# Performance work log

Hardware: AMD Instinct MI355X
Metric: run time of the kernel (lower is better)

The kernel has to match this reference:

```python
import jax, jax.numpy as jnp
import numpy as np

C_MSA, C_Z, C_HID, N_HEADS = 64, 128, 32, 8
INF = 1e8
EPS = 1e-5

def layer_norm(x, g, b):
    mu = jnp.mean(x, axis=-1, keepdims=True)
    var = jnp.var(x, axis=-1, keepdims=True)
    return (x - mu) * jax.lax.rsqrt(var + EPS) * g + b

def setup_inputs() -> dict:
    key = jax.random.key(0)
    ks = jax.random.split(key, 8)
    n_seq, n_res = 256, 512
    m = jax.random.normal(ks[0], (n_seq, n_res, C_MSA), dtype=jnp.float32)
    z = jax.random.normal(ks[1], (n_res, n_res, C_Z), dtype=jnp.float32)
    msa_mask = jnp.ones((n_seq, n_res), dtype=jnp.float32)
    z_mask = jnp.ones((n_res, n_res), dtype=jnp.float32)
    hc = N_HEADS * C_HID
    s_v = 1.0 / np.sqrt(C_MSA)
    W_v = jax.random.normal(ks[2], (hc, C_MSA), dtype=jnp.float32) * s_v
    W_g = jax.random.normal(ks[3], (hc, C_MSA), dtype=jnp.float32) * s_v  # 'gating' init is zeros; random for testing
    W_b = jax.random.normal(ks[4], (N_HEADS, C_Z), dtype=jnp.float32) * (1.0 / np.sqrt(C_Z))
    W_o = jax.random.normal(ks[5], (C_MSA, hc), dtype=jnp.float32) * (1.0 / np.sqrt(hc))
    ln_m_g = jnp.ones((C_MSA,), jnp.float32); ln_m_b = jnp.zeros((C_MSA,), jnp.float32)
    ln_z_g = jnp.ones((C_Z,), jnp.float32); ln_z_b = jnp.zeros((C_Z,), jnp.float32)
    return {"m": m, "z": z, "msa_mask": msa_mask, "z_mask": z_mask,
            "ln_m_g": ln_m_g, "ln_m_b": ln_m_b, "W_v": W_v, "W_g": W_g,
            "ln_z_g": ln_z_g, "ln_z_b": ln_z_b, "W_b": W_b, "W_o": W_o}

def reference(m, z, msa_mask, z_mask, ln_m_g, ln_m_b, W_v, W_g, ln_z_g, ln_z_b, W_b, W_o):
    n_seq, n_res, _ = m.shape
    m_ln = layer_norm(m, ln_m_g, ln_m_b)                      # [s, i, c_msa]
    v = (m_ln @ W_v.T).reshape(n_seq, n_res, N_HEADS, C_HID)  # [s, j, h, c]
    g = jax.nn.sigmoid(m_ln @ W_g.T).reshape(n_seq, n_res, N_HEADS, C_HID)
    b = layer_norm(z, ln_z_g, ln_z_b) @ W_b.T                 # [i, j, h]
    b = b + INF * (z_mask[..., None] - 1.0)
    v = v * msa_mask[..., None, None]
    w = jax.nn.softmax(b, axis=-2)                            # softmax over j
    # o[s,i,h,c] = sum_j v[s,j,h,c] * w[i,j,h]  (no broadcast materialization)
    o = g * jnp.einsum('sjhc,ijh->sihc', v, w)
    out = o.reshape(n_seq, n_res, N_HEADS * C_HID) @ W_o.T    # [s, i, c_msa]
    return out
```

## Files before the change

### kernel.cpp

```cpp
#include <hip/hip_runtime.h>
#include <stdint.h>


typedef unsigned short u16;
typedef unsigned int u32;
typedef __attribute__((ext_vector_type(4))) float f32x4;
typedef __attribute__((ext_vector_type(8))) short bf16x8;

#define INF8 1e8f

__device__ __forceinline__ u16 f2bf(float f) {
  u32 u = __float_as_uint(f);
  u = u + 0x7fffu + ((u >> 16) & 1u);
  return (u16)(u >> 16);
}
__device__ __forceinline__ float bf2f(u16 h) {
  return __uint_as_float(((u32)h) << 16);
}

#define GLD_LDS16(gp, lp) __builtin_amdgcn_global_load_lds(                 \
    (__attribute__((address_space(1))) const void*)(gp),                    \
    (__attribute__((address_space(3))) void*)(lp), 16, 0, 0)

__global__ __launch_bounds__(256) void k1_bias_softmax(
    const float* __restrict__ z, const float* __restrict__ z_mask,
    const float* __restrict__ gzp, const float* __restrict__ bzp,
    const float* __restrict__ W_b, u16* __restrict__ w_out)
{
  const int i = blockIdx.x;
  const int t = threadIdx.x;
  __shared__ float zn[32][133];
  __shared__ float bl[8][512];
  __shared__ float wb[8][128];
  __shared__ float gz[128], bz[128];
  for (int idx = t; idx < 1024; idx += 256) wb[idx >> 7][idx & 127] = W_b[idx];
  if (t < 128) { gz[t] = gzp[t]; bz[t] = bzp[t]; }
  __syncthreads();

  const int jl = t >> 3;
  const int part = t & 7;
  const int h = t >> 5, jj = t & 31;

  for (int chunk = 0; chunk < 16; ++chunk) {
    const float* zrow = z + ((size_t)i * 512 + chunk * 32 + jl) * 128;
    f32x4 v[4];
    float s = 0.f, sq = 0.f;
#pragma unroll
    for (int q = 0; q < 4; ++q) {
      v[q] = *reinterpret_cast<const f32x4*>(zrow + 4 * (part + 8 * q));
#pragma unroll
      for (int e = 0; e < 4; ++e) { s += v[q][e]; sq += v[q][e] * v[q][e]; }
    }
#pragma unroll
    for (int msk = 1; msk < 8; msk <<= 1) {
      s += __shfl_xor(s, msk, 8);
      sq += __shfl_xor(sq, msk, 8);
    }
    float mean = s * (1.f / 128.f);
    float rstd = rsqrtf(sq * (1.f / 128.f) - mean * mean + 1e-5f);
#pragma unroll
    for (int q = 0; q < 4; ++q) {
      int k0 = 4 * (part + 8 * q);
#pragma unroll
      for (int e = 0; e < 4; ++e) {
        int k = k0 + e;
        zn[jl][k] = (v[q][e] - mean) * rstd * gz[k] + bz[k];
      }
    }
    __syncthreads();
    {
      float acc = 0.f;
#pragma unroll 8
      for (int k = 0; k < 128; ++k) acc += zn[jj][k] * wb[h][k];
      float zm = z_mask[(size_t)i * 512 + chunk * 32 + jj];
      bl[h][chunk * 32 + jj] = acc + INF8 * (zm - 1.f);
    }
    __syncthreads();
  }
  {
    const int l = t & 31;
    float vals[16];
    float mx = -3.4e38f;
#pragma unroll
    for (int q = 0; q < 16; ++q) { vals[q] = bl[h][l + 32 * q]; mx = fmaxf(mx, vals[q]); }
#pragma unroll
    for (int msk = 1; msk < 32; msk <<= 1) mx = fmaxf(mx, __shfl_xor(mx, msk, 32));
    float sum = 0.f;
#pragma unroll
    for (int q = 0; q < 16; ++q) { vals[q] = __expf(vals[q] - mx); sum += vals[q]; }
#pragma unroll
    for (int msk = 1; msk < 32; msk <<= 1) sum += __shfl_xor(sum, msk, 32);
    float inv = 1.f / sum;
    u16* wrow = w_out + ((size_t)h * 512 + i) * 512;
#pragma unroll
    for (int q = 0; q < 16; ++q) wrow[l + 32 * q] = f2bf(vals[q] * inv);
  }
}

__global__ __launch_bounds__(256) void k2_vg(
    const float* __restrict__ m, const float* __restrict__ msa_mask,
    const float* __restrict__ gmp, const float* __restrict__ bmp,
    const float* __restrict__ W_v, const float* __restrict__ W_g,
    u16* __restrict__ vT, u16* __restrict__ g_out)
{
  const int jt = blockIdx.x, s = blockIdx.y;
  const int j0 = jt * 128;
  const int t = threadIdx.x;
  const int lane = t & 63, wid = t >> 6;
  __shared__ u16 bt[128][80];
  __shared__ float gk[64], bk[64];
  if (t < 64) { gk[t] = gmp[t]; bk[t] = bmp[t]; }
  __syncthreads();

  if (t < 128) {
    const float* mrow = m + ((size_t)s * 512 + j0 + t) * 64;
    f32x4 v[16];
    float s1 = 0.f, s2 = 0.f;
#pragma unroll
    for (int q = 0; q < 16; ++q) {
      v[q] = *reinterpret_cast<const f32x4*>(mrow + 4 * q);
#pragma unroll
      for (int e = 0; e < 4; ++e) { s1 += v[q][e]; s2 += v[q][e] * v[q][e]; }
    }
    float mean = s1 * (1.f / 64.f);
    float rstd = rsqrtf(s2 * (1.f / 64.f) - mean * mean + 1e-5f);
#pragma unroll
    for (int q = 0; q < 16; ++q) {
      int k0 = q * 4;
      u32 p0 = (u32)f2bf((v[q][0] - mean) * rstd * gk[k0]     + bk[k0])
             | ((u32)f2bf((v[q][1] - mean) * rstd * gk[k0 + 1] + bk[k0 + 1]) << 16);
      u32 p1 = (u32)f2bf((v[q][2] - mean) * rstd * gk[k0 + 2] + bk[k0 + 2])
             | ((u32)f2bf((v[q][3] - mean) * rstd * gk[k0 + 3] + bk[k0 + 3]) << 16);
      *reinterpret_cast<u32*>(&bt[t][k0]) = p0;
      *reinterpret_cast<u32*>(&bt[t][k0 + 2]) = p1;
    }
  }

  const float* Wsrc = (wid < 2) ? W_v : W_g;
  const int row0 = (wid & 1) * 128;
  const int r16 = lane & 15, kg = lane >> 4;
  bf16x8 afrag[8][2];
#pragma unroll
  for (int mf = 0; mf < 8; ++mf) {
    int row = row0 + mf * 16 + r16;
#pragma unroll
    for (int kf = 0; kf < 2; ++kf) {
      int k = kf * 32 + kg * 8;
      f32x4 x0 = *reinterpret_cast<const f32x4*>(Wsrc + row * 64 + k);
      f32x4 x1 = *reinterpret_cast<const f32x4*>(Wsrc + row * 64 + k + 4);
      bf16x8 a;
      a[0] = (short)f2bf(x0[0]); a[1] = (short)f2bf(x0[1]);
      a[2] = (short)f2bf(x0[2]); a[3] = (short)f2bf(x0[3]);
      a[4] = (short)f2bf(x1[0]); a[5] = (short)f2bf(x1[1]);
      a[6] = (short)f2bf(x1[2]); a[7] = (short)f2bf(x1[3]);
      afrag[mf][kf] = a;
    }
  }
  __syncthreads();

  for (int nc = 0; nc < 8; ++nc) {
    bf16x8 b0 = *reinterpret_cast<const bf16x8*>(&bt[nc * 16 + r16][kg * 8]);
    bf16x8 b1 = *reinterpret_cast<const bf16x8*>(&bt[nc * 16 + r16][32 + kg * 8]);
    f32x4 acc[8];
#pragma unroll
    for (int mf = 0; mf < 8; ++mf) acc[mf] = (f32x4){0.f, 0.f, 0.f, 0.f};
#pragma unroll
    for (int mf = 0; mf < 8; ++mf) {
      acc[mf] = __builtin_amdgcn_mfma_f32_16x16x32_bf16(afrag[mf][0], b0, acc[mf], 0, 0, 0);
      acc[mf] = __builtin_amdgcn_mfma_f32_16x16x32_bf16(afrag[mf][1], b1, acc[mf], 0, 0, 0);
    }
    const int colj = j0 + nc * 16 + r16;
    if (wid < 2) {
      float mask = msa_mask[(size_t)s * 512 + colj];
#pragma unroll
      for (int mf = 0; mf < 8; ++mf) {
#pragma unroll
        for (int r = 0; r < 4; ++r) {
          int hcrow = row0 + mf * 16 + kg * 4 + r;
          int hh = hcrow >> 5, cc = hcrow & 31;
          vT[((size_t)hh * 8192 + s * 32 + cc) * 512 + colj] = f2bf(acc[mf][r] * mask);
        }
      }
    } else {
#pragma unroll
      for (int mf = 0; mf < 8; ++mf) {
        int hcrow0 = row0 + mf * 16 + kg * 4;
        u16 pk0 = f2bf(1.f / (1.f + __expf(-acc[mf][0])));
        u16 pk1 = f2bf(1.f / (1.f + __expf(-acc[mf][1])));
        u16 pk2 = f2bf(1.f / (1.f + __expf(-acc[mf][2])));
        u16 pk3 = f2bf(1.f / (1.f + __expf(-acc[mf][3])));
        u32* dst = reinterpret_cast<u32*>(g_out + ((size_t)s * 512 + colj) * 256 + hcrow0);
        dst[0] = (u32)pk0 | ((u32)pk1 << 16);
        dst[1] = (u32)pk2 | ((u32)pk3 << 16);
      }
    }
  }
}

__global__ __launch_bounds__(256) void k3_einsum(
    const u16* __restrict__ w_buf, const u16* __restrict__ vT,
    float* __restrict__ O)
{
  const int nt = blockIdx.x, mt = blockIdx.y, h = blockIdx.z;
  const int t = threadIdx.x, lane = t & 63, wid = t >> 6;
  const int Mbase = mt * 128, Nbase = nt * 128;
  __shared__ u16 at[128 * 32];
  __shared__ u16 btl[128 * 32];
  const u16* Ag = w_buf + (size_t)h * 512 * 512;
  const u16* Bg = vT + (size_t)h * 8192 * 512;
  const int wr = wid >> 1, wc = wid & 1;
  const int r16 = lane & 15, kg = lane >> 4;
  const int srow = lane >> 2, scol = (lane & 3) * 8;
  f32x4 acc[4][4];
#pragma unroll
  for (int ii = 0; ii < 4; ++ii)
#pragma unroll
    for (int jj2 = 0; jj2 < 4; ++jj2) acc[ii][jj2] = (f32x4){0.f, 0.f, 0.f, 0.f};

  for (int kt = 0; kt < 16; ++kt) {
    const int k0 = kt * 32;
#pragma unroll
    for (int q = 0; q < 2; ++q) {
      const int rbase = wid * 32 + q * 16;
      GLD_LDS16(Ag + (size_t)(Mbase + rbase + srow) * 512 + k0 + scol, at + rbase * 32);
      GLD_LDS16(Bg + (size_t)(Nbase + rbase + srow) * 512 + k0 + scol, btl + rbase * 32);
    }
    __syncthreads();
    bf16x8 av[4], bv[4];
#pragma unroll
    for (int mf = 0; mf < 4; ++mf)
      av[mf] = *reinterpret_cast<const bf16x8*>(&at[(wr * 64 + mf * 16 + r16) * 32 + kg * 8]);
#pragma unroll
    for (int nf = 0; nf < 4; ++nf)
      bv[nf] = *reinterpret_cast<const bf16x8*>(&btl[(wc * 64 + nf * 16 + r16) * 32 + kg * 8]);
#pragma unroll
    for (int mf = 0; mf < 4; ++mf)
#pragma unroll
      for (int nf = 0; nf < 4; ++nf)
        acc[mf][nf] = __builtin_amdgcn_mfma_f32_16x16x32_bf16(av[mf], bv[nf], acc[mf][nf], 0, 0, 0);
    __syncthreads();
  }
  float* Obase = O + (size_t)h * 512 * 8192;
#pragma unroll
  for (int mf = 0; mf < 4; ++mf) {
#pragma unroll
    for (int r = 0; r < 4; ++r) {
      const int irow = Mbase + wr * 64 + mf * 16 + kg * 4 + r;
#pragma unroll
      for (int nf = 0; nf < 4; ++nf) {
        const int n = Nbase + wc * 64 + nf * 16 + r16;
        Obase[(size_t)irow * 8192 + n] = acc[mf][nf][r];
      }
    }
  }
}

__global__ __launch_bounds__(256) void k4_out(
    const float* __restrict__ O, const u16* __restrict__ g_buf,
    const float* __restrict__ W_o, float* __restrict__ out)
{
  const int st = blockIdx.x, i = blockIdx.y;
  const int s0 = st * 64;
  const int t = threadIdx.x, lane = t & 63, wid = t >> 6;
  __shared__ u16 Al[64][264];
  __shared__ u16 Wl[64][264];
  for (int idx = t; idx < 64 * 256; idx += 256) {
    int row = idx >> 8, col = idx & 255;
    Wl[row][col] = f2bf(W_o[idx]);
  }
  {
    const int hh = t >> 5, cc = t & 31;
    const float* Op = O + ((size_t)hh * 512 + i) * 8192 + (size_t)s0 * 32 + cc;
    const u16* gp = g_buf + ((size_t)s0 * 512 + i) * 256 + t;
#pragma unroll 4
    for (int sl = 0; sl < 64; ++sl) {
      float ov = Op[sl * 32];
      float gv = bf2f(gp[sl * 131072]);
      Al[sl][t] = f2bf(ov * gv);
    }
  }
  __syncthreads();

  const int r16 = lane & 15, kg = lane >> 4;
  f32x4 acc[4];
#pragma unroll
  for (int nf = 0; nf < 4; ++nf) acc[nf] = (f32x4){0.f, 0.f, 0.f, 0.f};
#pragma unroll
  for (int kf = 0; kf < 8; ++kf) {
    bf16x8 a = *reinterpret_cast<const bf16x8*>(&Al[wid * 16 + r16][kf * 32 + kg * 8]);
#pragma unroll
    for (int nf = 0; nf < 4; ++nf) {
      bf16x8 b = *reinterpret_cast<const bf16x8*>(&Wl[nf * 16 + r16][kf * 32 + kg * 8]);
      acc[nf] = __builtin_amdgcn_mfma_f32_16x16x32_bf16(a, b, acc[nf], 0, 0, 0);
    }
  }
#pragma unroll
  for (int nf = 0; nf < 4; ++nf) {
#pragma unroll
    for (int r = 0; r < 4; ++r) {
      int srow = wid * 16 + kg * 4 + r;
      int cm = nf * 16 + r16;
      out[((size_t)(s0 + srow) * 512 + i) * 64 + cm] = acc[nf][r];
    }
  }
}

extern "C" void kernel_launch(void* const* d_in, const int* in_sizes, int n_in,
                              void* d_out, int out_size, void* d_ws, size_t ws_size,
                              hipStream_t stream) {
  const float* m        = (const float*)d_in[0];
  const float* z        = (const float*)d_in[1];
  const float* msa_mask = (const float*)d_in[2];
  const float* z_mask   = (const float*)d_in[3];
  const float* ln_m_g   = (const float*)d_in[4];
  const float* ln_m_b   = (const float*)d_in[5];
  const float* W_v      = (const float*)d_in[6];
  const float* W_g      = (const float*)d_in[7];
  const float* ln_z_g   = (const float*)d_in[8];
  const float* ln_z_b   = (const float*)d_in[9];
  const float* W_b      = (const float*)d_in[10];
  const float* W_o      = (const float*)d_in[11];
  float* out = (float*)d_out;

  char* ws = (char*)d_ws;
  u16*   w_buf = (u16*)(ws);
  u16*   vT    = (u16*)(ws + (4u << 20));
  u16*   g_buf = (u16*)(ws + (68u << 20));
  float* O     = (float*)(ws + (132u << 20));

  k1_bias_softmax<<<dim3(512), dim3(256), 0, stream>>>(z, z_mask, ln_z_g, ln_z_b, W_b, w_buf);
  k2_vg<<<dim3(4, 256), dim3(256), 0, stream>>>(m, msa_mask, ln_m_g, ln_m_b, W_v, W_g, vT, g_buf);
  k3_einsum<<<dim3(64, 4, 8), dim3(256), 0, stream>>>(w_buf, vT, O);
  k4_out<<<dim3(4, 512), dim3(256), 0, stream>>>(O, g_buf, W_o, out);
}
```

Before: 438.4 us.

## Rewrite pipeline with MFMA bias, bf16 intermediate O, swizzled LDS and coalesced stores

Replaces nearly every kernel. Weights are pre-converted to bf16 once, and the z-bias projection moves to MFMA in a separate kernel followed by a standalone softmax. The v/g projection stages its transposed output through LDS so global stores are coalesced. The einsum uses K=64 tiles with XOR-swizzled LDS and writes O as bf16 in an [i,s,hc] layout so the output kernel can read it contiguously. This cuts the fp32 O traffic and the strided scattered accesses, at the cost of extra launches, an fp32 bias round trip, and more bf16 rounding of O.

```diff
diff --git a/kernel.cpp b/kernel.cpp
--- a/kernel.cpp
+++ b/kernel.cpp
@@ -7,281 +7,381 @@
 typedef __attribute__((ext_vector_type(4))) float f32x4;
 typedef __attribute__((ext_vector_type(8))) short bf16x8;
 
-#define INF8 1e8f
-
 __device__ __forceinline__ u16 f2bf(float f) {
   u32 u = __float_as_uint(f);
   u = u + 0x7fffu + ((u >> 16) & 1u);
   return (u16)(u >> 16);
 }
-__device__ __forceinline__ float bf2f(u16 h) {
-  return __uint_as_float(((u32)h) << 16);
+__device__ __forceinline__ float bf2f(u16 h) { return __uint_as_float(((u32)h) << 16); }
+
+__device__ __forceinline__ bf16x8 pack8(const float* f) {
+  bf16x8 r;
+#pragma unroll
+  for (int e = 0; e < 8; ++e) r[e] = (short)f2bf(f[e]);
+  return r;
 }
 
 #define GLD_LDS16(gp, lp) __builtin_amdgcn_global_load_lds(                 \
     (__attribute__((address_space(1))) const void*)(gp),                    \
     (__attribute__((address_space(3))) void*)(lp), 16, 0, 0)
 
-__global__ __launch_bounds__(256) void k1_bias_softmax(
+__global__ __launch_bounds__(256) void k0_convert(
+    const float* __restrict__ W_v, const float* __restrict__ W_g,
+    const float* __restrict__ W_o, const float* __restrict__ W_b,
+    u16* __restrict__ Wvg, u16* __restrict__ Wo, u16* __restrict__ Wb)
+{
+  int id = blockIdx.x * 256 + threadIdx.x;
+  if (id < 32768) {
+    int row = id >> 6, col = id & 63;
+    float v = (row < 256) ? W_v[row * 64 + col] : W_g[(row - 256) * 64 + col];
+    Wvg[id] = f2bf(v);
+  } else if (id < 49152) {
+    int k = id - 32768;
+    Wo[k] = f2bf(W_o[k]);
+  } else if (id < 51200) {
+    int k = id - 49152;
+    Wb[k] = (k < 1024) ? f2bf(W_b[k]) : (u16)0;
+  }
+}
+
+__global__ __launch_bounds__(256) void k1a_bias(
     const float* __restrict__ z, const float* __restrict__ z_mask,
     const float* __restrict__ gzp, const float* __restrict__ bzp,
-    const float* __restrict__ W_b, u16* __restrict__ w_out)
-{
-  const int i = blockIdx.x;
-  const int t = threadIdx.x;
-  __shared__ float zn[32][133];
-  __shared__ float bl[8][512];
-  __shared__ float wb[8][128];
+    const u16* __restrict__ Wb, float* __restrict__ bbuf)
+{
+  const int jc = blockIdx.x, i = blockIdx.y;
+  const int j0 = jc * 128;
+  const int t = threadIdx.x, lane = t & 63, wid = t >> 6;
+  const int r16 = lane & 15, kg = lane >> 4;
+  __shared__ char zns[32768];
+  __shared__ float bl[8][132];
   __shared__ float gz[128], bz[128];
-  for (int idx = t; idx < 1024; idx += 256) wb[idx >> 7][idx & 127] = W_b[idx];
   if (t < 128) { gz[t] = gzp[t]; bz[t] = bzp[t]; }
   __syncthreads();
 
-  const int jl = t >> 3;
-  const int part = t & 7;
-  const int h = t >> 5, jj = t & 31;
-
-  for (int chunk = 0; chunk < 16; ++chunk) {
-    const float* zrow = z + ((size_t)i * 512 + chunk * 32 + jl) * 128;
-    f32x4 v[4];
+#pragma unroll
+  for (int rr = 0; rr < 2; ++rr) {
+    const int row = rr * 64 + (t >> 2), part = t & 3;
+    const float* zr = z + ((size_t)i * 512 + j0 + row) * 128 + part * 32;
+    f32x4 v[8];
     float s = 0.f, sq = 0.f;
 #pragma unroll
-    for (int q = 0; q < 4; ++q) {
-      v[q] = *reinterpret_cast<const f32x4*>(zrow + 4 * (part + 8 * q));
+    for (int q = 0; q < 8; ++q) {
+      v[q] = *reinterpret_cast<const f32x4*>(zr + 4 * q);
 #pragma unroll
       for (int e = 0; e < 4; ++e) { s += v[q][e]; sq += v[q][e] * v[q][e]; }
     }
-#pragma unroll
-    for (int msk = 1; msk < 8; msk <<= 1) {
-      s += __shfl_xor(s, msk, 8);
-      sq += __shfl_xor(sq, msk, 8);
-    }
+    s += __shfl_xor(s, 1); s += __shfl_xor(s, 2);
+    sq += __shfl_xor(sq, 1); sq += __shfl_xor(sq, 2);
     float mean = s * (1.f / 128.f);
     float rstd = rsqrtf(sq * (1.f / 128.f) - mean * mean + 1e-5f);
 #pragma unroll
-    for (int q = 0; q < 4; ++q) {
-      int k0 = 4 * (part + 8 * q);
-#pragma unroll
-      for (int e = 0; e < 4; ++e) {
-        int k = k0 + e;
-        zn[jl][k] = (v[q][e] - mean) * rstd * gz[k] + bz[k];
+    for (int uu = 0; uu < 4; ++uu) {
+      float tmp[8];
+#pragma unroll
+      for (int e = 0; e < 8; ++e) {
+        int k = part * 32 + uu * 8 + e;
+        tmp[e] = (v[uu * 2 + (e >> 2)][e & 3] - mean) * rstd * gz[k] + bz[k];
       }
-    }
-    __syncthreads();
-    {
-      float acc = 0.f;
-#pragma unroll 8
-      for (int k = 0; k < 128; ++k) acc += zn[jj][k] * wb[h][k];
-      float zm = z_mask[(size_t)i * 512 + chunk * 32 + jj];
-      bl[h][chunk * 32 + jj] = acc + INF8 * (zm - 1.f);
-    }
-    __syncthreads();
-  }
+      int byte = (row * 256 + part * 64 + uu * 16) ^ ((row & 7) << 4);
+      *reinterpret_cast<bf16x8*>(zns + byte) = pack8(tmp);
+    }
+  }
+  __syncthreads();
+
+  bf16x8 av[2][4], bw[4];
+#pragma unroll
+  for (int mf = 0; mf < 2; ++mf)
+#pragma unroll
+    for (int kf = 0; kf < 4; ++kf) {
+      int row = wid * 32 + mf * 16 + r16;
+      int byte = (row * 256 + (kf * 4 + kg) * 16) ^ ((row & 7) << 4);
+      av[mf][kf] = *reinterpret_cast<const bf16x8*>(zns + byte);
+    }
+#pragma unroll
+  for (int kf = 0; kf < 4; ++kf)
+    bw[kf] = *reinterpret_cast<const bf16x8*>(Wb + r16 * 128 + kf * 32 + kg * 8);
+  f32x4 acc[2];
+  acc[0] = (f32x4){0.f, 0.f, 0.f, 0.f}; acc[1] = acc[0];
+#pragma unroll
+  for (int mf = 0; mf < 2; ++mf)
+#pragma unroll
+    for (int kf = 0; kf < 4; ++kf)
+      acc[mf] = __builtin_amdgcn_mfma_f32_16x16x32_bf16(av[mf][kf], bw[kf], acc[mf], 0, 0, 0);
+  if (r16 < 8) {
+#pragma unroll
+    for (int mf = 0; mf < 2; ++mf)
+#pragma unroll
+      for (int r = 0; r < 4; ++r)
+        bl[r16][wid * 32 + mf * 16 + kg * 4 + r] = acc[mf][r];
+  }
+  __syncthreads();
+
   {
-    const int l = t & 31;
-    float vals[16];
-    float mx = -3.4e38f;
-#pragma unroll
-    for (int q = 0; q < 16; ++q) { vals[q] = bl[h][l + 32 * q]; mx = fmaxf(mx, vals[q]); }
-#pragma unroll
-    for (int msk = 1; msk < 32; msk <<= 1) mx = fmaxf(mx, __shfl_xor(mx, msk, 32));
-    float sum = 0.f;
-#pragma unroll
-    for (int q = 0; q < 16; ++q) { vals[q] = __expf(vals[q] - mx); sum += vals[q]; }
-#pragma unroll
-    for (int msk = 1; msk < 32; msk <<= 1) sum += __shfl_xor(sum, msk, 32);
-    float inv = 1.f / sum;
-    u16* wrow = w_out + ((size_t)h * 512 + i) * 512;
-#pragma unroll
-    for (int q = 0; q < 16; ++q) wrow[l + 32 * q] = f2bf(vals[q] * inv);
-  }
-}
-
-__global__ __launch_bounds__(256) void k2_vg(
+    const int h = t >> 5, jj = t & 31;
+    f32x4 bv = *reinterpret_cast<const f32x4*>(&bl[h][jj * 4]);
+    f32x4 zm = *reinterpret_cast<const f32x4*>(z_mask + (size_t)i * 512 + j0 + jj * 4);
+#pragma unroll
+    for (int e = 0; e < 4; ++e) bv[e] += 1e8f * (zm[e] - 1.f);
+    *reinterpret_cast<f32x4*>(bbuf + ((size_t)h * 512 + i) * 512 + j0 + jj * 4) = bv;
+  }
+}
+
+__global__ __launch_bounds__(256) void k1b_softmax(
+    const float* __restrict__ bbuf, u16* __restrict__ wbuf)
+{
+  const int t = threadIdx.x, lane = t & 63, wid = t >> 6;
+  const size_t row = (size_t)blockIdx.x * 4 + wid;
+  const float* src = bbuf + row * 512 + lane * 8;
+  f32x4 a = *reinterpret_cast<const f32x4*>(src);
+  f32x4 b = *reinterpret_cast<const f32x4*>(src + 4);
+  float vals[8];
+#pragma unroll
+  for (int e = 0; e < 4; ++e) { vals[e] = a[e]; vals[4 + e] = b[e]; }
+  float mx = vals[0];
+#pragma unroll
+  for (int e = 1; e < 8; ++e) mx = fmaxf(mx, vals[e]);
+#pragma unroll
+  for (int m = 1; m < 64; m <<= 1) mx = fmaxf(mx, __shfl_xor(mx, m));
+  float sum = 0.f;
+#pragma unroll
+  for (int e = 0; e < 8; ++e) { vals[e] = __expf(vals[e] - mx); sum += vals[e]; }
+#pragma unroll
+  for (int m = 1; m < 64; m <<= 1) sum += __shfl_xor(sum, m);
+  float inv = 1.f / sum;
+  bf16x8 o;
+#pragma unroll
+  for (int e = 0; e < 8; ++e) o[e] = (short)f2bf(vals[e] * inv);
+  *reinterpret_cast<bf16x8*>(wbuf + row * 512 + lane * 8) = o;
+}
+
+__global__ __launch_bounds__(512) void k2_vg(
     const float* __restrict__ m, const float* __restrict__ msa_mask,
     const float* __restrict__ gmp, const float* __restrict__ bmp,
-    const float* __restrict__ W_v, const float* __restrict__ W_g,
-    u16* __restrict__ vT, u16* __restrict__ g_out)
+    const u16* __restrict__ Wvg, u16* __restrict__ vT, u16* __restrict__ gbuf)
 {
   const int jt = blockIdx.x, s = blockIdx.y;
   const int j0 = jt * 128;
-  const int t = threadIdx.x;
-  const int lane = t & 63, wid = t >> 6;
-  __shared__ u16 bt[128][80];
-  __shared__ float gk[64], bk[64];
-  if (t < 64) { gk[t] = gmp[t]; bk[t] = bmp[t]; }
-  __syncthreads();
-
-  if (t < 128) {
-    const float* mrow = m + ((size_t)s * 512 + j0 + t) * 64;
-    f32x4 v[16];
-    float s1 = 0.f, s2 = 0.f;
-#pragma unroll
-    for (int q = 0; q < 16; ++q) {
-      v[q] = *reinterpret_cast<const f32x4*>(mrow + 4 * q);
-#pragma unroll
-      for (int e = 0; e < 4; ++e) { s1 += v[q][e]; s2 += v[q][e] * v[q][e]; }
-    }
-    float mean = s1 * (1.f / 64.f);
-    float rstd = rsqrtf(s2 * (1.f / 64.f) - mean * mean + 1e-5f);
-#pragma unroll
-    for (int q = 0; q < 16; ++q) {
-      int k0 = q * 4;
-      u32 p0 = (u32)f2bf((v[q][0] - mean) * rstd * gk[k0]     + bk[k0])
-             | ((u32)f2bf((v[q][1] - mean) * rstd * gk[k0 + 1] + bk[k0 + 1]) << 16);
-      u32 p1 = (u32)f2bf((v[q][2] - mean) * rstd * gk[k0 + 2] + bk[k0 + 2])
-             | ((u32)f2bf((v[q][3] - mean) * rstd * gk[k0 + 3] + bk[k0 + 3]) << 16);
-      *reinterpret_cast<u32*>(&bt[t][k0]) = p0;
-      *reinterpret_cast<u32*>(&bt[t][k0 + 2]) = p1;
-    }
-  }
-
-  const float* Wsrc = (wid < 2) ? W_v : W_g;
-  const int row0 = (wid & 1) * 128;
+  const int t = threadIdx.x, lane = t & 63, wid = t >> 6;
   const int r16 = lane & 15, kg = lane >> 4;
-  bf16x8 afrag[8][2];
-#pragma unroll
-  for (int mf = 0; mf < 8; ++mf) {
-    int row = row0 + mf * 16 + r16;
+  __shared__ char smem[65536];
+  __shared__ float maskl[128], gk[64], bk[64];
+  if (t < 64) gk[t] = gmp[t];
+  else if (t < 128) bk[t - 64] = bmp[t - 64];
+  if (t < 128) maskl[t] = msa_mask[(size_t)s * 512 + j0 + t];
+  __syncthreads();
+
+  {
+    const int row = t >> 2, part = t & 3;
+    const float* mr = m + ((size_t)s * 512 + j0 + row) * 64 + part * 16;
+    f32x4 v[4];
+    float sm = 0.f, sq = 0.f;
+#pragma unroll
+    for (int q = 0; q < 4; ++q) {
+      v[q] = *reinterpret_cast<const f32x4*>(mr + 4 * q);
+#pragma unroll
+      for (int e = 0; e < 4; ++e) { sm += v[q][e]; sq += v[q][e] * v[q][e]; }
+    }
+    sm += __shfl_xor(sm, 1); sm += __shfl_xor(sm, 2);
+    sq += __shfl_xor(sq, 1); sq += __shfl_xor(sq, 2);
+    float mean = sm * (1.f / 64.f);
+    float rstd = rsqrtf(sq * (1.f / 64.f) - mean * mean + 1e-5f);
+#pragma unroll
+    for (int uu = 0; uu < 2; ++uu) {
+      float tmp[8];
+#pragma unroll
+      for (int e = 0; e < 8; ++e) {
+        int k = part * 16 + uu * 8 + e;
+        tmp[e] = (v[uu * 2 + (e >> 2)][e & 3] - mean) * rstd * gk[k] + bk[k];
+      }
+      int byte = (row * 128 + part * 32 + uu * 16) ^ ((row & 7) << 4);
+      *reinterpret_cast<bf16x8*>(smem + byte) = pack8(tmp);
+    }
+  }
+  __syncthreads();
+
+  const int jh = wid & 1, hcq0 = wid >> 1;
+  bf16x8 av[4][2];
+#pragma unroll
+  for (int mf = 0; mf < 4; ++mf)
 #pragma unroll
     for (int kf = 0; kf < 2; ++kf) {
-      int k = kf * 32 + kg * 8;
-      f32x4 x0 = *reinterpret_cast<const f32x4*>(Wsrc + row * 64 + k);
-      f32x4 x1 = *reinterpret_cast<const f32x4*>(Wsrc + row * 64 + k + 4);
-      bf16x8 a;
-      a[0] = (short)f2bf(x0[0]); a[1] = (short)f2bf(x0[1]);
-      a[2] = (short)f2bf(x0[2]); a[3] = (short)f2bf(x0[3]);
-      a[4] = (short)f2bf(x1[0]); a[5] = (short)f2bf(x1[1]);
-      a[6] = (short)f2bf(x1[2]); a[7] = (short)f2bf(x1[3]);
-      afrag[mf][kf] = a;
-    }
-  }
-  __syncthreads();
-
-  for (int nc = 0; nc < 8; ++nc) {
-    bf16x8 b0 = *reinterpret_cast<const bf16x8*>(&bt[nc * 16 + r16][kg * 8]);
-    bf16x8 b1 = *reinterpret_cast<const bf16x8*>(&bt[nc * 16 + r16][32 + kg * 8]);
-    f32x4 acc[8];
-#pragma unroll
-    for (int mf = 0; mf < 8; ++mf) acc[mf] = (f32x4){0.f, 0.f, 0.f, 0.f};
-#pragma unroll
-    for (int mf = 0; mf < 8; ++mf) {
-      acc[mf] = __builtin_amdgcn_mfma_f32_16x16x32_bf16(afrag[mf][0], b0, acc[mf], 0, 0, 0);
-      acc[mf] = __builtin_amdgcn_mfma_f32_16x16x32_bf16(afrag[mf][1], b1, acc[mf], 0, 0, 0);
-    }
-    const int colj = j0 + nc * 16 + r16;
-    if (wid < 2) {
-      float mask = msa_mask[(size_t)s * 512 + colj];
-#pragma unroll
-      for (int mf = 0; mf < 8; ++mf) {
-#pragma unroll
-        for (int r = 0; r < 4; ++r) {
-          int hcrow = row0 + mf * 16 + kg * 4 + r;
-          int hh = hcrow >> 5, cc = hcrow & 31;
-          vT[((size_t)hh * 8192 + s * 32 + cc) * 512 + colj] = f2bf(acc[mf][r] * mask);
-        }
+      int row = jh * 64 + mf * 16 + r16;
+      int byte = (row * 128 + (kf * 4 + kg) * 16) ^ ((row & 7) << 4);
+      av[mf][kf] = *reinterpret_cast<const bf16x8*>(smem + byte);
+    }
+  __syncthreads();
+
+#pragma unroll
+  for (int rep = 0; rep < 2; ++rep) {
+    const int hcq = hcq0 + rep * 4;
+    bf16x8 bv[4][2];
+#pragma unroll
+    for (int nf = 0; nf < 4; ++nf)
+#pragma unroll
+      for (int kf = 0; kf < 2; ++kf)
+        bv[nf][kf] = *reinterpret_cast<const bf16x8*>(
+            Wvg + (hcq * 64 + nf * 16 + r16) * 64 + kf * 32 + kg * 8);
+    f32x4 acc[4][4];
+#pragma unroll
+    for (int mf = 0; mf < 4; ++mf)
+#pragma unroll
+      for (int nf = 0; nf < 4; ++nf) acc[mf][nf] = (f32x4){0.f, 0.f, 0.f, 0.f};
+#pragma unroll
+    for (int mf = 0; mf < 4; ++mf)
+#pragma unroll
+      for (int nf = 0; nf < 4; ++nf)
+#pragma unroll
+        for (int kf = 0; kf < 2; ++kf)
+          acc[mf][nf] = __builtin_amdgcn_mfma_f32_16x16x32_bf16(av[mf][kf], bv[nf][kf], acc[mf][nf], 0, 0, 0);
+
+    if (rep == 0) {
+#pragma unroll
+      for (int mf = 0; mf < 4; ++mf)
+#pragma unroll
+        for (int nf = 0; nf < 4; ++nf)
+#pragma unroll
+          for (int r = 0; r < 4; ++r) {
+            int j = jh * 64 + mf * 16 + kg * 4 + r;
+            int hc = hcq * 64 + nf * 16 + r16;
+            float val = acc[mf][nf][r] * maskl[j];
+            int byte = (hc * 256 + j * 2) ^ ((hc & 7) << 4);
+            *reinterpret_cast<u16*>(smem + byte) = f2bf(val);
+          }
+      __syncthreads();
+#pragma unroll
+      for (int it = 0; it < 8; ++it) {
+        int u = it * 512 + t;
+        int hc = u >> 4, sub = u & 15;
+        int byte = (hc * 256 + sub * 16) ^ ((hc & 7) << 4);
+        bf16x8 rv = *reinterpret_cast<const bf16x8*>(smem + byte);
+        int h = hc >> 5, c = hc & 31;
+        *reinterpret_cast<bf16x8*>(
+            vT + (((size_t)h * 8192 + s * 32 + c) * 512 + j0 + sub * 8)) = rv;
       }
     } else {
 #pragma unroll
-      for (int mf = 0; mf < 8; ++mf) {
-        int hcrow0 = row0 + mf * 16 + kg * 4;
-        u16 pk0 = f2bf(1.f / (1.f + __expf(-acc[mf][0])));
-        u16 pk1 = f2bf(1.f / (1.f + __expf(-acc[mf][1])));
-        u16 pk2 = f2bf(1.f / (1.f + __expf(-acc[mf][2])));
-        u16 pk3 = f2bf(1.f / (1.f + __expf(-acc[mf][3])));
-        u32* dst = reinterpret_cast<u32*>(g_out + ((size_t)s * 512 + colj) * 256 + hcrow0);
-        dst[0] = (u32)pk0 | ((u32)pk1 << 16);
-        dst[1] = (u32)pk2 | ((u32)pk3 << 16);
-      }
+      for (int mf = 0; mf < 4; ++mf)
+#pragma unroll
+        for (int nf = 0; nf < 4; ++nf)
+#pragma unroll
+          for (int r = 0; r < 4; ++r) {
+            int j = jh * 64 + mf * 16 + kg * 4 + r;
+            int hc = hcq0 * 64 + nf * 16 + r16;
+            float val = 1.f / (1.f + __expf(-acc[mf][nf][r]));
+            gbuf[((size_t)s * 512 + j0 + j) * 256 + hc] = f2bf(val);
+          }
     }
   }
 }
 
 __global__ __launch_bounds__(256) void k3_einsum(
-    const u16* __restrict__ w_buf, const u16* __restrict__ vT,
-    float* __restrict__ O)
+    const u16* __restrict__ wbuf, const u16* __restrict__ vT, u16* __restrict__ O2)
 {
   const int nt = blockIdx.x, mt = blockIdx.y, h = blockIdx.z;
   const int t = threadIdx.x, lane = t & 63, wid = t >> 6;
   const int Mbase = mt * 128, Nbase = nt * 128;
-  __shared__ u16 at[128 * 32];
-  __shared__ u16 btl[128 * 32];
-  const u16* Ag = w_buf + (size_t)h * 512 * 512;
-  const u16* Bg = vT + (size_t)h * 8192 * 512;
+  __shared__ char smem[32768];
+  const u16* Ag = wbuf + (size_t)h * 262144;
+  const u16* Bg = vT + (size_t)h * 4194304;
   const int wr = wid >> 1, wc = wid & 1;
   const int r16 = lane & 15, kg = lane >> 4;
-  const int srow = lane >> 2, scol = (lane & 3) * 8;
+  const int lrow = lane >> 3, lslot = lane & 7;
   f32x4 acc[4][4];
 #pragma unroll
-  for (int ii = 0; ii < 4; ++ii)
-#pragma unroll
-    for (int jj2 = 0; jj2 < 4; ++jj2) acc[ii][jj2] = (f32x4){0.f, 0.f, 0.f, 0.f};
-
-  for (int kt = 0; kt < 16; ++kt) {
-    const int k0 = kt * 32;
-#pragma unroll
-    for (int q = 0; q < 2; ++q) {
-      const int rbase = wid * 32 + q * 16;
-      GLD_LDS16(Ag + (size_t)(Mbase + rbase + srow) * 512 + k0 + scol, at + rbase * 32);
-      GLD_LDS16(Bg + (size_t)(Nbase + rbase + srow) * 512 + k0 + scol, btl + rbase * 32);
+  for (int a = 0; a < 4; ++a)
+#pragma unroll
+    for (int b = 0; b < 4; ++b) acc[a][b] = (f32x4){0.f, 0.f, 0.f, 0.f};
+
+  for (int kt = 0; kt < 8; ++kt) {
+    const int k0 = kt * 64;
+#pragma unroll
+    for (int q = 0; q < 4; ++q) {
+      const int rb = wid * 32 + q * 8;
+      const int pr = rb + lrow;
+      const int su = (lslot ^ (pr & 7)) * 8;
+      GLD_LDS16(Ag + (size_t)(Mbase + pr) * 512 + k0 + su, (u16*)smem + rb * 64);
+      GLD_LDS16(Bg + (size_t)(Nbase + pr) * 512 + k0 + su, (u16*)(smem + 16384) + rb * 64);
     }
     __syncthreads();
-    bf16x8 av[4], bv[4];
+    bf16x8 av[4][2], bv[4][2];
 #pragma unroll
     for (int mf = 0; mf < 4; ++mf)
-      av[mf] = *reinterpret_cast<const bf16x8*>(&at[(wr * 64 + mf * 16 + r16) * 32 + kg * 8]);
+#pragma unroll
+      for (int kf = 0; kf < 2; ++kf) {
+        int rowA = wr * 64 + mf * 16 + r16;
+        int byteA = (rowA * 128 + (kf * 4 + kg) * 16) ^ ((rowA & 7) << 4);
+        av[mf][kf] = *reinterpret_cast<const bf16x8*>(smem + byteA);
+        int rowB = wc * 64 + mf * 16 + r16;
+        int byteB = (rowB * 128 + (kf * 4 + kg) * 16) ^ ((rowB & 7) << 4);
+        bv[mf][kf] = *reinterpret_cast<const bf16x8*>(smem + 16384 + byteB);
+      }
+#pragma unroll
+    for (int mf = 0; mf < 4; ++mf)
+#pragma unroll
+      for (int nf = 0; nf < 4; ++nf)
+#pragma unroll
+        for (int kf = 0; kf < 2; ++kf)
+          acc[mf][nf] = __builtin_amdgcn_mfma_f32_16x16x32_bf16(av[mf][kf], bv[nf][kf], acc[mf][nf], 0, 0, 0);
+    __syncthreads();
+  }
+
+  u16* Tep = (u16*)smem;
+#pragma unroll
+  for (int mf = 0; mf < 4; ++mf)
 #pragma unroll
     for (int nf = 0; nf < 4; ++nf)
-      bv[nf] = *reinterpret_cast<const bf16x8*>(&btl[(wc * 64 + nf * 16 + r16) * 32 + kg * 8]);
-#pragma unroll
-    for (int mf = 0; mf < 4; ++mf)
-#pragma unroll
-      for (int nf = 0; nf < 4; ++nf)
-        acc[mf][nf] = __builtin_amdgcn_mfma_f32_16x16x32_bf16(av[mf], bv[nf], acc[mf][nf], 0, 0, 0);
-    __syncthreads();
-  }
-  float* Obase = O + (size_t)h * 512 * 8192;
-#pragma unroll
-  for (int mf = 0; mf < 4; ++mf) {
-#pragma unroll
-    for (int r = 0; r < 4; ++r) {
-      const int irow = Mbase + wr * 64 + mf * 16 + kg * 4 + r;
-#pragma unroll
-      for (int nf = 0; nf < 4; ++nf) {
-        const int n = Nbase + wc * 64 + nf * 16 + r16;
-        Obase[(size_t)irow * 8192 + n] = acc[mf][nf][r];
+#pragma unroll
+      for (int r = 0; r < 4; ++r) {
+        int il = wr * 64 + mf * 16 + kg * 4 + r;
+        int sc = wc * 64 + nf * 16 + r16;
+        Tep[il * 128 + sc] = f2bf(acc[mf][nf][r]);
       }
-    }
+  __syncthreads();
+#pragma unroll
+  for (int it = 0; it < 8; ++it) {
+    int u = it * 256 + t;
+    int il = u >> 4, sub = u & 15;
+    bf16x8 rv = *reinterpret_cast<const bf16x8*>(Tep + il * 128 + sub * 8);
+    int scg = Nbase + sub * 8;
+    int sI = scg >> 5, c = scg & 31;
+    *reinterpret_cast<bf16x8*>(
+        O2 + (((size_t)(Mbase + il) * 256 + sI) * 256 + h * 32 + c)) = rv;
   }
 }
 
 __global__ __launch_bounds__(256) void k4_out(
-    const float* __restrict__ O, const u16* __restrict__ g_buf,
-    const float* __restrict__ W_o, float* __restrict__ out)
+    const u16* __restrict__ O2, const u16* __restrict__ gbuf,
+    const u16* __restrict__ Wo, float* __restrict__ out)
 {
   const int st = blockIdx.x, i = blockIdx.y;
   const int s0 = st * 64;
   const int t = threadIdx.x, lane = t & 63, wid = t >> 6;
+  const int r16 = lane & 15, kg = lane >> 4;
   __shared__ u16 Al[64][264];
   __shared__ u16 Wl[64][264];
-  for (int idx = t; idx < 64 * 256; idx += 256) {
-    int row = idx >> 8, col = idx & 255;
-    Wl[row][col] = f2bf(W_o[idx]);
+#pragma unroll
+  for (int it = 0; it < 8; ++it) {
+    int u = it * 256 + t, row = u >> 5, sub = u & 31;
+    *reinterpret_cast<bf16x8*>(&Wl[row][sub * 8]) =
+        *reinterpret_cast<const bf16x8*>(Wo + row * 256 + sub * 8);
   }
   {
-    const int hh = t >> 5, cc = t & 31;
-    const float* Op = O + ((size_t)hh * 512 + i) * 8192 + (size_t)s0 * 32 + cc;
-    const u16* gp = g_buf + ((size_t)s0 * 512 + i) * 256 + t;
-#pragma unroll 4
-    for (int sl = 0; sl < 64; ++sl) {
-      float ov = Op[sl * 32];
-      float gv = bf2f(gp[sl * 131072]);
-      Al[sl][t] = f2bf(ov * gv);
-    }
-  }
-  __syncthreads();
-
-  const int r16 = lane & 15, kg = lane >> 4;
+    const int sl = t >> 2, hc0 = (t & 3) * 64;
+    const u16* Op = O2 + ((size_t)i * 256 + s0 + sl) * 256 + hc0;
+    const u16* gp = gbuf + ((size_t)(s0 + sl) * 512 + i) * 256 + hc0;
+#pragma unroll
+    for (int uu = 0; uu < 8; ++uu) {
+      bf16x8 ov = *reinterpret_cast<const bf16x8*>(Op + uu * 8);
+      bf16x8 gv = *reinterpret_cast<const bf16x8*>(gp + uu * 8);
+      bf16x8 r;
+#pragma unroll
+      for (int e = 0; e < 8; ++e) r[e] = (short)f2bf(bf2f((u16)ov[e]) * bf2f((u16)gv[e]));
+      *reinterpret_cast<bf16x8*>(&Al[sl][hc0 + uu * 8]) = r;
+    }
+  }
+  __syncthreads();
+
   f32x4 acc[4];
 #pragma unroll
   for (int nf = 0; nf < 4; ++nf) acc[nf] = (f32x4){0.f, 0.f, 0.f, 0.f};
@@ -295,14 +395,10 @@
     }
   }
 #pragma unroll
-  for (int nf = 0; nf < 4; ++nf) {
-#pragma unroll
-    for (int r = 0; r < 4; ++r) {
-      int srow = wid * 16 + kg * 4 + r;
-      int cm = nf * 16 + r16;
-      out[((size_t)(s0 + srow) * 512 + i) * 64 + cm] = acc[nf][r];
-    }
-  }
+  for (int nf = 0; nf < 4; ++nf)
+#pragma unroll
+    for (int r = 0; r < 4; ++r)
+      out[((size_t)(s0 + wid * 16 + kg * 4 + r) * 512 + i) * 64 + nf * 16 + r16] = acc[nf][r];
 }
 
 extern "C" void kernel_launch(void* const* d_in, const int* in_sizes, int n_in,
@@ -323,13 +419,19 @@
   float* out = (float*)d_out;
 
   char* ws = (char*)d_ws;
-  u16*   w_buf = (u16*)(ws);
-  u16*   vT    = (u16*)(ws + (4u << 20));
-  u16*   g_buf = (u16*)(ws + (68u << 20));
-  float* O     = (float*)(ws + (132u << 20));
-
-  k1_bias_softmax<<<dim3(512), dim3(256), 0, stream>>>(z, z_mask, ln_z_g, ln_z_b, W_b, w_buf);
-  k2_vg<<<dim3(4, 256), dim3(256), 0, stream>>>(m, msa_mask, ln_m_g, ln_m_b, W_v, W_g, vT, g_buf);
-  k3_einsum<<<dim3(64, 4, 8), dim3(256), 0, stream>>>(w_buf, vT, O);
-  k4_out<<<dim3(4, 512), dim3(256), 0, stream>>>(O, g_buf, W_o, out);
-}
+  u16*   Wvg  = (u16*)(ws);
+  u16*   Wo   = (u16*)(ws + 65536);
+  u16*   Wb   = (u16*)(ws + 98304);
+  float* bbuf = (float*)(ws + (1u  << 20));
+  u16*   wbuf = (u16*)  (ws + (9u  << 20));
+  u16*   vT   = (u16*)  (ws + (16u << 20));
+  u16*   gbuf = (u16*)  (ws + (80u << 20));
+  u16*   O2   = (u16*)  (ws + (144u << 20));
+
+  k0_convert<<<200, 256, 0, stream>>>(W_v, W_g, W_o, W_b, Wvg, Wo, Wb);
+  k1a_bias<<<dim3(4, 512), 256, 0, stream>>>(z, z_mask, ln_z_g, ln_z_b, Wb, bbuf);
+  k1b_softmax<<<1024, 256, 0, stream>>>(bbuf, wbuf);
+  k2_vg<<<dim3(4, 256), 512, 0, stream>>>(m, msa_mask, ln_m_g, ln_m_b, Wvg, vT, gbuf);
+  k3_einsum<<<dim3(64, 4, 8), 256, 0, stream>>>(wbuf, vT, O2);
+  k4_out<<<dim3(4, 512), 256, 0, stream>>>(O2, gbuf, Wo, out);
+}
```

After: 379.8 us. -13.4%, faster.
